# Kernel tuning notes

Measured on AMD Instinct MI355X. Metric: run time of the kernel, lower is better.

The kernel has to match this reference:

```python
import jax, jax.numpy as jnp
import numpy as np
from jax import lax

C = 256

def conv1x1(x, w, b):
    # x: [B,C,H,W], w: [O,C], b: [O]
    return jnp.einsum('bchw,oc->bohw', x, w) + b[None, :, None, None]

def conv3x3_s2(x, w, b):
    # x: [B,C,H,W], w: [O,C,3,3] -> stride 2, pad 1
    y = lax.conv_general_dilated(x, w, window_strides=(2, 2),
                                 padding=((1, 1), (1, 1)),
                                 dimension_numbers=('NCHW', 'OIHW', 'NCHW'))
    return y + b[None, :, None, None]

def to_qv(x):
    # [B,C,H,W] -> permute(0,2,3,1) -> view [B,H,W,1,C]
    return jnp.transpose(x, (0, 2, 3, 1))[:, :, :, None, :]

def to_k(x):
    # [B,C,H,W] -> permute(0,2,3,1) -> view [B,H,W,C,1]
    return jnp.transpose(x, (0, 2, 3, 1))[:, :, :, :, None]

def upsample2x_nearest(x):
    return jnp.repeat(jnp.repeat(x, 2, axis=2), 2, axis=3)


def setup_inputs() -> dict:
    key = jax.random.key(0)
    ks = jax.random.split(key, 20)
    x1 = jax.random.normal(ks[0], (2, C, 128, 128), dtype=jnp.float32)
    x2 = jax.random.normal(ks[1], (2, C, 64, 64), dtype=jnp.float32)
    s = 0.05
    d = {'x1': x1, 'x2': x2}
    names = ['q1', 'q2', 'ks1', 'ks2', 'kup', 'v1', 'v2']
    for i, n in enumerate(names):
        d[n + '_w'] = jax.random.normal(ks[2 + 2 * i], (C, C), dtype=jnp.float32) * s
        d[n + '_b'] = jax.random.normal(ks[3 + 2 * i], (C,), dtype=jnp.float32) * s
    d['kdown_w'] = jax.random.normal(ks[16], (C, C, 3, 3), dtype=jnp.float32) * s
    d['kdown_b'] = jax.random.normal(ks[17], (C,), dtype=jnp.float32) * s
    return d


def reference(x1, x2, q1_w, q1_b, q2_w, q2_b, ks1_w, ks1_b, ks2_w, ks2_b,
              kup_w, kup_b, v1_w, v1_b, v2_w, v2_b, kdown_w, kdown_b):
    q1 = to_qv(conv1x1(x1, q1_w, q1_b))            # [B,128,128,1,C]
    q2 = to_qv(conv1x1(x2, q2_w, q2_b))            # [B,64,64,1,C]
    k_up = to_k(upsample2x_nearest(conv1x1(x2, kup_w, kup_b)))  # [B,128,128,C,1]
    k_self_1 = to_k(conv1x1(x1, ks1_w, ks1_b))     # [B,128,128,C,1]
    k_self_2 = to_k(conv1x1(x2, ks2_w, ks2_b))     # [B,64,64,C,1]
    k_down = to_k(conv3x3_s2(x1, kdown_w, kdown_b))  # [B,64,64,C,1]
    v1 = to_qv(conv1x1(x1, v1_w, v1_b))            # [B,128,128,1,C]
    v2 = to_qv(conv1x1(x2, v2_w, v2_b))            # [B,64,64,1,C]
    return (q1, q2, k_up, k_self_1, k_self_2, k_down, v1, v2)
```

## Files before the change

### kernel.cpp

```cpp
#include <hip/hip_runtime.h>
#include <hip/hip_bf16.h>
#include <stdint.h>


typedef __attribute__((ext_vector_type(8))) __bf16 bf16x8;
typedef __attribute__((ext_vector_type(4))) float f32x4;

typedef const __attribute__((address_space(1))) uint32_t* gptr_t;
typedef __attribute__((address_space(3))) uint32_t* lptr_t;

__device__ __forceinline__ void cp16(void* lds, const void* g) {
  gptr_t gp = reinterpret_cast<gptr_t>(reinterpret_cast<uintptr_t>(g));
  lptr_t lp = reinterpret_cast<lptr_t>(
      static_cast<uint32_t>(reinterpret_cast<uintptr_t>(lds)));
  __builtin_amdgcn_global_load_lds(gp, lp, 16, 0, 0);
}

__global__ void nchw2nhwc_bf16(const float* __restrict__ src,
                               uint16_t* __restrict__ dst,
                               int H, int W, int pad) {
  __shared__ float tile[64][65];
  const int tid = threadIdx.x;
  const int tx = tid & 63;
  const int tg = tid >> 6;
  const int b = blockIdx.z / H;
  const int h = blockIdx.z - b * H;
  const int wt = blockIdx.x * 64;
  const int ct = blockIdx.y * 64;
  const float* s = src + ((long)(b * 256 + ct) * H + h) * W + wt;
  const long cstride = (long)H * W;
#pragma unroll
  for (int i = 0; i < 16; i++) {
    const int cl = tg * 16 + i;
    tile[cl][tx] = s[(long)cl * cstride + tx];
  }
  __syncthreads();
  const int Wp = W + 2 * pad;
  __hip_bfloat16* d = reinterpret_cast<__hip_bfloat16*>(dst);
  const long dbase =
      (((long)(b * (H + 2 * pad) + h + pad)) * Wp + pad + wt) * 256 + ct + tx;
#pragma unroll
  for (int j = 0; j < 16; j++) {
    const int wl = tg * 16 + j;
    d[dbase + (long)wl * 256] = __float2bfloat16(tile[tx][wl]);
  }
}

struct WArgs {
  const float* w1[7];
  const float* kdw;
};

__global__ void convert_weights(WArgs a, uint16_t* __restrict__ wb,
                                uint16_t* __restrict__ wt) {
  const int idx = blockIdx.x * 256 + threadIdx.x;
  if (idx < 7 * 65536) {
    const int which = idx >> 16;
    reinterpret_cast<__hip_bfloat16*>(wb)[idx] =
        __float2bfloat16(a.w1[which][idx & 65535]);
  }
  if (idx < 9 * 65536) {
    const int tap = idx >> 16;
    const int o = (idx >> 8) & 255;
    const int c = idx & 255;
    reinterpret_cast<__hip_bfloat16*>(wt)[idx] =
        __float2bfloat16(a.kdw[o * 2304 + c * 9 + tap]);
  }
}

struct Job {
  const uint16_t* A;
  const uint16_t* W;
  const float* bias;
  float* out;
  int mtiles;
  int mode;
};
struct JobArgs {
  Job j[8];
};

__global__ __launch_bounds__(256, 2) void fused_gemm(JobArgs args) {
  const Job jb = args.j[blockIdx.z];
  if ((int)blockIdx.x >= jb.mtiles) return;
  const int mtile = blockIdx.x;
  const int ntile = blockIdx.y;
  const int mode = jb.mode;

  __shared__ __align__(16) uint16_t lA[128 * 32];
  __shared__ __align__(16) uint16_t lB[128 * 32];

  const int tid = threadIdx.x;
  const int lane = tid & 63;
  const int wave = tid >> 6;
  const int wr = wave & 1;
  const int wc = wave >> 1;

  const int cid0 = wave * 128 + lane;
  const int cid1 = cid0 + 64;
  const int rA0 = cid0 >> 2, kc0 = cid0 & 3;
  const int rA1 = cid1 >> 2, kc1 = cid1 & 3;

  long abase0, abase1;
  {
    const int m0 = mtile * 128 + rA0;
    const int m1 = mtile * 128 + rA1;
    if (mode == 0) {
      abase0 = ((long)((m0 >> 14) * 130 + ((m0 >> 7) & 127) + 1) * 130 +
                (m0 & 127) + 1) * 256;
      abase1 = ((long)((m1 >> 14) * 130 + ((m1 >> 7) & 127) + 1) * 130 +
                (m1 & 127) + 1) * 256;
    } else if (mode == 3) {
      abase0 = ((long)((m0 >> 12) * 130 + 2 * ((m0 >> 6) & 63)) * 130 +
                2 * (m0 & 63)) * 256;
      abase1 = ((long)((m1 >> 12) * 130 + 2 * ((m1 >> 6) & 63)) * 130 +
                2 * (m1 & 63)) * 256;
    } else {
      abase0 = (long)m0 * 256;
      abase1 = (long)m1 * 256;
    }
  }
  const uint16_t* pa0 = jb.A + abase0 + kc0 * 8;
  const uint16_t* pa1 = jb.A + abase1 + kc1 * 8;
  const uint16_t* pb0 = jb.W + (long)(ntile * 128 + rA0) * 256 + kc0 * 8;
  const uint16_t* pb1 = jb.W + (long)(ntile * 128 + rA1) * 256 + kc1 * 8;

  uint16_t* dA0 = lA + wave * 1024;
  uint16_t* dA1 = dA0 + 512;
  uint16_t* dB0 = lB + wave * 1024;
  uint16_t* dB1 = dB0 + 512;

  const int q = lane >> 4;
  const int l15 = lane & 15;
  const uint16_t* ra[4];
  const uint16_t* rb[4];
#pragma unroll
  for (int i = 0; i < 4; i++) {
    ra[i] = lA + (wr * 64 + i * 16 + l15) * 32 + q * 8;
    rb[i] = lB + (wc * 64 + i * 16 + l15) * 32 + q * 8;
  }

  f32x4 acc[4][4] = {};

  auto step = [&](int ks, bool conv) {
    long aoff, woff;
    if (conv) {
      const int tap = ks >> 3;
      const int k0 = (ks & 7) * 32;
      const int kh = tap / 3;
      const int kw = tap - kh * 3;
      aoff = (long)(kh * 130 + kw) * 256 + k0;
      woff = (long)tap * 65536 + k0;
    } else {
      aoff = woff = (long)ks * 32;
    }
    __syncthreads();
    cp16(dA0, pa0 + aoff);
    cp16(dA1, pa1 + aoff);
    cp16(dB0, pb0 + woff);
    cp16(dB1, pb1 + woff);
    __syncthreads();
    bf16x8 af[4], bfr[4];
#pragma unroll
    for (int i = 0; i < 4; i++) af[i] = *(const bf16x8*)ra[i];
#pragma unroll
    for (int i = 0; i < 4; i++) bfr[i] = *(const bf16x8*)rb[i];
#pragma unroll
    for (int i = 0; i < 4; i++)
#pragma unroll
      for (int j = 0; j < 4; j++)
        acc[i][j] = __builtin_amdgcn_mfma_f32_16x16x32_bf16(af[i], bfr[j],
                                                            acc[i][j], 0, 0, 0);
  };

  if (mode == 3) {
    for (int ks = 0; ks < 72; ks++) step(ks, true);
  } else {
#pragma unroll
    for (int ks = 0; ks < 8; ks++) step(ks, false);
  }

  const int nbase = ntile * 128 + wc * 64 + l15;
  const int mbase = mtile * 128 + wr * 64 + q * 4;
#pragma unroll
  for (int j = 0; j < 4; j++) {
    const int n = nbase + j * 16;
    const float bv = jb.bias[n];
#pragma unroll
    for (int i = 0; i < 4; i++) {
      const int m0 = mbase + i * 16;
      const f32x4 v = acc[i][j];
      if (mode == 2) {
#pragma unroll
        for (int r = 0; r < 4; r++) {
          const int m = m0 + r;
          const int b = m >> 12;
          const int h2 = (m >> 6) & 63;
          const int w2 = m & 63;
          const float val = v[r] + bv;
          float* o = jb.out + ((long)(b * 128 + 2 * h2) * 128 + 2 * w2) * 256 + n;
          o[0] = val;
          o[256] = val;
          o[32768] = val;
          o[32768 + 256] = val;
        }
      } else {
#pragma unroll
        for (int r = 0; r < 4; r++) {
          jb.out[(long)(m0 + r) * 256 + n] = v[r] + bv;
        }
      }
    }
  }
}

extern "C" void kernel_launch(void* const* d_in, const int* in_sizes, int n_in,
                              void* d_out, int out_size, void* d_ws,
                              size_t ws_size, hipStream_t stream) {
  (void)in_sizes; (void)n_in; (void)out_size; (void)ws_size;
  const float* x1 = (const float*)d_in[0];
  const float* x2 = (const float*)d_in[1];
  float* out = (float*)d_out;

  uint16_t* x1p = (uint16_t*)d_ws;
  uint16_t* x2b = x1p + 8652800;
  uint16_t* wb = x2b + 2097152;
  uint16_t* wt = wb + 7 * 65536;

  hipMemsetAsync(x1p, 0, 8652800 * sizeof(uint16_t), stream);
  nchw2nhwc_bf16<<<dim3(2, 4, 256), 256, 0, stream>>>(x1, x1p, 128, 128, 1);
  nchw2nhwc_bf16<<<dim3(1, 4, 128), 256, 0, stream>>>(x2, x2b, 64, 64, 0);

  WArgs wa;
  wa.w1[0] = (const float*)d_in[2];
  wa.w1[1] = (const float*)d_in[4];
  wa.w1[2] = (const float*)d_in[6];
  wa.w1[3] = (const float*)d_in[8];
  wa.w1[4] = (const float*)d_in[10];
  wa.w1[5] = (const float*)d_in[12];
  wa.w1[6] = (const float*)d_in[14];
  wa.kdw = (const float*)d_in[16];
  convert_weights<<<2304, 256, 0, stream>>>(wa, wb, wt);

  JobArgs ja;
  ja.j[0] = {x1p, wt,             (const float*)d_in[17], out + 29360128L, 64, 3};
  ja.j[1] = {x1p, wb + 0 * 65536, (const float*)d_in[3],  out + 0L,        256, 0};
  ja.j[2] = {x1p, wb + 2 * 65536, (const float*)d_in[7],  out + 18874368L, 256, 0};
  ja.j[3] = {x1p, wb + 5 * 65536, (const float*)d_in[13], out + 31457280L, 256, 0};
  ja.j[4] = {x2b, wb + 4 * 65536, (const float*)d_in[11], out + 10485760L, 64, 2};
  ja.j[5] = {x2b, wb + 1 * 65536, (const float*)d_in[5],  out + 8388608L,  64, 1};
  ja.j[6] = {x2b, wb + 3 * 65536, (const float*)d_in[9],  out + 27262976L, 64, 1};
  ja.j[7] = {x2b, wb + 6 * 65536, (const float*)d_in[15], out + 39845888L, 64, 1};
  fused_gemm<<<dim3(256, 2, 8), 256, 0, stream>>>(ja);
}
```

Measured before the change: 297.3 us.

## Restructure GEMM to full-N tiles with fragment-packed weights and split-K conv

The GEMM kernel now computes a full 256-wide N tile per block, staging the whole 128x256 A tile in LDS once per tap. It reads B straight from global memory in a weight layout pre-packed into MFMA fragment order, which drops the per-32-K double barrier loop. The 3x3 stride-2 conv is split across three jobs of three taps each that atomically accumulate into an output zeroed beforehand, evening out the per-block work. The transpose and weight-conversion kernels are also vectorised with float4 loads and 16-byte stores. The cost is twice the accumulator registers and 64KB of LDS, which may lower occupancy, plus fp32 atomics on the conv output.

```diff
diff --git a/kernel.cpp b/kernel.cpp
--- a/kernel.cpp
+++ b/kernel.cpp
@@ -5,6 +5,7 @@
 
 typedef __attribute__((ext_vector_type(8))) __bf16 bf16x8;
 typedef __attribute__((ext_vector_type(4))) float f32x4;
+typedef __attribute__((ext_vector_type(8))) unsigned short u16x8;
 
 typedef const __attribute__((address_space(1))) uint32_t* gptr_t;
 typedef __attribute__((address_space(3))) uint32_t* lptr_t;
@@ -16,33 +17,43 @@
   __builtin_amdgcn_global_load_lds(gp, lp, 16, 0, 0);
 }
 
-__global__ void nchw2nhwc_bf16(const float* __restrict__ src,
-                               uint16_t* __restrict__ dst,
-                               int H, int W, int pad) {
+__global__ void nchw2nhwc_v2(const float* __restrict__ src,
+                             uint16_t* __restrict__ dst,
+                             int H, int W, int pad) {
   __shared__ float tile[64][65];
   const int tid = threadIdx.x;
-  const int tx = tid & 63;
-  const int tg = tid >> 6;
   const int b = blockIdx.z / H;
   const int h = blockIdx.z - b * H;
   const int wt = blockIdx.x * 64;
   const int ct = blockIdx.y * 64;
+  const long cs = (long)H * W;
   const float* s = src + ((long)(b * 256 + ct) * H + h) * W + wt;
-  const long cstride = (long)H * W;
-#pragma unroll
-  for (int i = 0; i < 16; i++) {
-    const int cl = tg * 16 + i;
-    tile[cl][tx] = s[(long)cl * cstride + tx];
+  const int rw = tid >> 4;
+  const int rf = tid & 15;
+#pragma unroll
+  for (int p = 0; p < 4; p++) {
+    const int cl = p * 16 + rw;
+    const float4 v = *(const float4*)(s + (long)cl * cs + rf * 4);
+    tile[cl][rf * 4 + 0] = v.x;
+    tile[cl][rf * 4 + 1] = v.y;
+    tile[cl][rf * 4 + 2] = v.z;
+    tile[cl][rf * 4 + 3] = v.w;
   }
   __syncthreads();
+  const int wl0 = tid >> 3;
+  const int cg = tid & 7;
   const int Wp = W + 2 * pad;
-  __hip_bfloat16* d = reinterpret_cast<__hip_bfloat16*>(dst);
-  const long dbase =
-      (((long)(b * (H + 2 * pad) + h + pad)) * Wp + pad + wt) * 256 + ct + tx;
-#pragma unroll
-  for (int j = 0; j < 16; j++) {
-    const int wl = tg * 16 + j;
-    d[dbase + (long)wl * 256] = __float2bfloat16(tile[tx][wl]);
+  const long rowb = ((long)(b * (H + 2 * pad) + h + pad)) * Wp + pad + wt;
+#pragma unroll
+  for (int p = 0; p < 2; p++) {
+    const int wl = p * 32 + wl0;
+    u16x8 u;
+#pragma unroll
+    for (int k = 0; k < 8; k++) {
+      __hip_bfloat16 hb = __float2bfloat16(tile[cg * 8 + k][wl]);
+      u[k] = *reinterpret_cast<uint16_t*>(&hb);
+    }
+    *(u16x8*)(dst + (rowb + wl) * 256 + ct + cg * 8) = u;
   }
 }
 
@@ -51,164 +62,172 @@
   const float* kdw;
 };
 
-__global__ void convert_weights(WArgs a, uint16_t* __restrict__ wb,
-                                uint16_t* __restrict__ wt) {
+__global__ void convert_weights_v2(WArgs a, uint16_t* __restrict__ wf) {
   const int idx = blockIdx.x * 256 + threadIdx.x;
-  if (idx < 7 * 65536) {
-    const int which = idx >> 16;
-    reinterpret_cast<__hip_bfloat16*>(wb)[idx] =
-        __float2bfloat16(a.w1[which][idx & 65535]);
-  }
-  if (idx < 9 * 65536) {
-    const int tap = idx >> 16;
-    const int o = (idx >> 8) & 255;
-    const int c = idx & 255;
-    reinterpret_cast<__hip_bfloat16*>(wt)[idx] =
-        __float2bfloat16(a.kdw[o * 2304 + c * 9 + tap]);
-  }
+  const int mat = idx >> 13;
+  const int g = idx & 8191;
+  const int jg = g >> 9;
+  const int kc = (g >> 6) & 7;
+  const int lane = g & 63;
+  const int o = jg * 16 + (lane & 15);
+  const int k0 = kc * 32 + (lane >> 4) * 8;
+  float f[8];
+  if (mat < 7) {
+    const float* w = a.w1[mat];
+    const float4 v0 = *(const float4*)(w + o * 256 + k0);
+    const float4 v1 = *(const float4*)(w + o * 256 + k0 + 4);
+    f[0] = v0.x; f[1] = v0.y; f[2] = v0.z; f[3] = v0.w;
+    f[4] = v1.x; f[5] = v1.y; f[6] = v1.z; f[7] = v1.w;
+  } else {
+    const int tap = mat - 7;
+#pragma unroll
+    for (int e = 0; e < 8; e++)
+      f[e] = a.kdw[(long)o * 2304 + (long)(k0 + e) * 9 + tap];
+  }
+  u16x8 u;
+#pragma unroll
+  for (int e = 0; e < 8; e++) {
+    __hip_bfloat16 hb = __float2bfloat16(f[e]);
+    u[e] = *reinterpret_cast<uint16_t*>(&hb);
+  }
+  *(u16x8*)(wf + (long)idx * 8) = u;
 }
 
 struct Job {
   const uint16_t* A;
-  const uint16_t* W;
+  const uint16_t* Wf;
   const float* bias;
   float* out;
   int mtiles;
   int mode;
+  int tap0;
 };
 struct JobArgs {
-  Job j[8];
+  Job j[10];
 };
 
 __global__ __launch_bounds__(256, 2) void fused_gemm(JobArgs args) {
   const Job jb = args.j[blockIdx.z];
   if ((int)blockIdx.x >= jb.mtiles) return;
   const int mtile = blockIdx.x;
-  const int ntile = blockIdx.y;
   const int mode = jb.mode;
 
-  __shared__ __align__(16) uint16_t lA[128 * 32];
-  __shared__ __align__(16) uint16_t lB[128 * 32];
+  __shared__ __align__(16) uint16_t lA[32768];
 
   const int tid = threadIdx.x;
   const int lane = tid & 63;
   const int wave = tid >> 6;
   const int wr = wave & 1;
   const int wc = wave >> 1;
-
-  const int cid0 = wave * 128 + lane;
-  const int cid1 = cid0 + 64;
-  const int rA0 = cid0 >> 2, kc0 = cid0 & 3;
-  const int rA1 = cid1 >> 2, kc1 = cid1 & 3;
-
-  long abase0, abase1;
-  {
-    const int m0 = mtile * 128 + rA0;
-    const int m1 = mtile * 128 + rA1;
-    if (mode == 0) {
-      abase0 = ((long)((m0 >> 14) * 130 + ((m0 >> 7) & 127) + 1) * 130 +
-                (m0 & 127) + 1) * 256;
-      abase1 = ((long)((m1 >> 14) * 130 + ((m1 >> 7) & 127) + 1) * 130 +
-                (m1 & 127) + 1) * 256;
-    } else if (mode == 3) {
-      abase0 = ((long)((m0 >> 12) * 130 + 2 * ((m0 >> 6) & 63)) * 130 +
-                2 * (m0 & 63)) * 256;
-      abase1 = ((long)((m1 >> 12) * 130 + 2 * ((m1 >> 6) & 63)) * 130 +
-                2 * (m1 & 63)) * 256;
-    } else {
-      abase0 = (long)m0 * 256;
-      abase1 = (long)m1 * 256;
-    }
-  }
-  const uint16_t* pa0 = jb.A + abase0 + kc0 * 8;
-  const uint16_t* pa1 = jb.A + abase1 + kc1 * 8;
-  const uint16_t* pb0 = jb.W + (long)(ntile * 128 + rA0) * 256 + kc0 * 8;
-  const uint16_t* pb1 = jb.W + (long)(ntile * 128 + rA1) * 256 + kc1 * 8;
-
-  uint16_t* dA0 = lA + wave * 1024;
-  uint16_t* dA1 = dA0 + 512;
-  uint16_t* dB0 = lB + wave * 1024;
-  uint16_t* dB1 = dB0 + 512;
-
   const int q = lane >> 4;
   const int l15 = lane & 15;
-  const uint16_t* ra[4];
-  const uint16_t* rb[4];
-#pragma unroll
-  for (int i = 0; i < 4; i++) {
-    ra[i] = lA + (wr * 64 + i * 16 + l15) * 32 + q * 8;
-    rb[i] = lB + (wc * 64 + i * 16 + l15) * 32 + q * 8;
-  }
-
-  f32x4 acc[4][4] = {};
-
-  auto step = [&](int ks, bool conv) {
-    long aoff, woff;
-    if (conv) {
-      const int tap = ks >> 3;
-      const int k0 = (ks & 7) * 32;
+
+  const uint16_t* rowA[2];
+  {
+    const int rbase = wave * 16 + (lane >> 2);
+#pragma unroll
+    for (int rh = 0; rh < 2; rh++) {
+      const int m = mtile * 128 + rh * 64 + rbase;
+      long p;
+      if (mode == 0) {
+        p = ((long)((m >> 14) * 130 + ((m >> 7) & 127) + 1)) * 130 + (m & 127) + 1;
+      } else if (mode == 3) {
+        p = ((long)((m >> 12) * 130 + 2 * ((m >> 6) & 63))) * 130 + 2 * (m & 63);
+      } else {
+        p = m;
+      }
+      rowA[rh] = jb.A + p * 256 + (lane & 3) * 8;
+    }
+  }
+
+  f32x4 acc[4][8] = {};
+  const int ntaps = (mode == 3) ? 3 : 1;
+
+  for (int t = 0; t < ntaps; t++) {
+    long aoff = 0;
+    const uint16_t* wf = jb.Wf;
+    if (mode == 3) {
+      const int tap = jb.tap0 + t;
       const int kh = tap / 3;
       const int kw = tap - kh * 3;
-      aoff = (long)(kh * 130 + kw) * 256 + k0;
-      woff = (long)tap * 65536 + k0;
-    } else {
-      aoff = woff = (long)ks * 32;
+      aoff = (long)(kh * 130 + kw) * 256;
+      wf = jb.Wf + (long)tap * 65536;
+    }
+    if (t) __syncthreads();
+#pragma unroll
+    for (int kap = 0; kap < 16; kap++) {
+      const uint16_t* src = rowA[kap & 1] + aoff + (kap >> 1) * 32;
+      cp16(lA + (kap * 256 + wave * 64) * 8, src);
     }
     __syncthreads();
-    cp16(dA0, pa0 + aoff);
-    cp16(dA1, pa1 + aoff);
-    cp16(dB0, pb0 + woff);
-    cp16(dB1, pb1 + woff);
-    __syncthreads();
-    bf16x8 af[4], bfr[4];
-#pragma unroll
-    for (int i = 0; i < 4; i++) af[i] = *(const bf16x8*)ra[i];
-#pragma unroll
-    for (int i = 0; i < 4; i++) bfr[i] = *(const bf16x8*)rb[i];
-#pragma unroll
-    for (int i = 0; i < 4; i++)
-#pragma unroll
-      for (int j = 0; j < 4; j++)
-        acc[i][j] = __builtin_amdgcn_mfma_f32_16x16x32_bf16(af[i], bfr[j],
-                                                            acc[i][j], 0, 0, 0);
-  };
-
+
+#pragma unroll
+    for (int kc = 0; kc < 8; kc++) {
+      bf16x8 av[4];
+#pragma unroll
+      for (int i = 0; i < 4; i++)
+        av[i] = *(const bf16x8*)(lA + (kc * 128 + wr * 64 + i * 16 + l15) * 32 + q * 8);
+#pragma unroll
+      for (int j = 0; j < 8; j++) {
+        const bf16x8 bv =
+            *(const bf16x8*)(wf + ((long)((wc * 8 + j) * 8 + kc) * 64 + lane) * 8);
+#pragma unroll
+        for (int i = 0; i < 4; i++)
+          acc[i][j] = __builtin_amdgcn_mfma_f32_16x16x32_bf16(av[i], bv,
+                                                              acc[i][j], 0, 0, 0);
+      }
+    }
+  }
+
+  const int nb = wc * 128 + l15;
+  const int mb = mtile * 128 + wr * 64 + q * 4;
   if (mode == 3) {
-    for (int ks = 0; ks < 72; ks++) step(ks, true);
-  } else {
-#pragma unroll
-    for (int ks = 0; ks < 8; ks++) step(ks, false);
-  }
-
-  const int nbase = ntile * 128 + wc * 64 + l15;
-  const int mbase = mtile * 128 + wr * 64 + q * 4;
-#pragma unroll
-  for (int j = 0; j < 4; j++) {
-    const int n = nbase + j * 16;
-    const float bv = jb.bias[n];
-#pragma unroll
-    for (int i = 0; i < 4; i++) {
-      const int m0 = mbase + i * 16;
-      const f32x4 v = acc[i][j];
-      if (mode == 2) {
+#pragma unroll
+    for (int j = 0; j < 8; j++) {
+      const int n = nb + j * 16;
+      const float bv = jb.bias ? jb.bias[n] : 0.0f;
+#pragma unroll
+      for (int i = 0; i < 4; i++) {
+        const int m0 = mb + i * 16;
+#pragma unroll
+        for (int r = 0; r < 4; r++)
+          atomicAdd(jb.out + (long)(m0 + r) * 256 + n, acc[i][j][r] + bv);
+      }
+    }
+  } else if (mode == 2) {
+#pragma unroll
+    for (int j = 0; j < 8; j++) {
+      const int n = nb + j * 16;
+      const float bv = jb.bias[n];
+#pragma unroll
+      for (int i = 0; i < 4; i++) {
+        const int m0 = mb + i * 16;
 #pragma unroll
         for (int r = 0; r < 4; r++) {
           const int m = m0 + r;
           const int b = m >> 12;
           const int h2 = (m >> 6) & 63;
           const int w2 = m & 63;
-          const float val = v[r] + bv;
+          const float val = acc[i][j][r] + bv;
           float* o = jb.out + ((long)(b * 128 + 2 * h2) * 128 + 2 * w2) * 256 + n;
           o[0] = val;
           o[256] = val;
           o[32768] = val;
           o[32768 + 256] = val;
         }
-      } else {
-#pragma unroll
-        for (int r = 0; r < 4; r++) {
-          jb.out[(long)(m0 + r) * 256 + n] = v[r] + bv;
-        }
+      }
+    }
+  } else {
+#pragma unroll
+    for (int j = 0; j < 8; j++) {
+      const int n = nb + j * 16;
+      const float bv = jb.bias[n];
+#pragma unroll
+      for (int i = 0; i < 4; i++) {
+        const int m0 = mb + i * 16;
+#pragma unroll
+        for (int r = 0; r < 4; r++)
+          jb.out[(long)(m0 + r) * 256 + n] = acc[i][j][r] + bv;
       }
     }
   }
@@ -224,12 +243,13 @@
 
   uint16_t* x1p = (uint16_t*)d_ws;
   uint16_t* x2b = x1p + 8652800;
-  uint16_t* wb = x2b + 2097152;
-  uint16_t* wt = wb + 7 * 65536;
+  uint16_t* wf = x2b + 2097152;
 
   hipMemsetAsync(x1p, 0, 8652800 * sizeof(uint16_t), stream);
-  nchw2nhwc_bf16<<<dim3(2, 4, 256), 256, 0, stream>>>(x1, x1p, 128, 128, 1);
-  nchw2nhwc_bf16<<<dim3(1, 4, 128), 256, 0, stream>>>(x2, x2b, 64, 64, 0);
+  hipMemsetAsync(out + 29360128L, 0, 2097152 * sizeof(float), stream);
+
+  nchw2nhwc_v2<<<dim3(2, 4, 256), 256, 0, stream>>>(x1, x1p, 128, 128, 1);
+  nchw2nhwc_v2<<<dim3(1, 4, 128), 256, 0, stream>>>(x2, x2b, 64, 64, 0);
 
   WArgs wa;
   wa.w1[0] = (const float*)d_in[2];
@@ -240,16 +260,19 @@
   wa.w1[5] = (const float*)d_in[12];
   wa.w1[6] = (const float*)d_in[14];
   wa.kdw = (const float*)d_in[16];
-  convert_weights<<<2304, 256, 0, stream>>>(wa, wb, wt);
-
+  convert_weights_v2<<<512, 256, 0, stream>>>(wa, wf);
+
+  const uint16_t* wfk = wf + 7 * 65536;
   JobArgs ja;
-  ja.j[0] = {x1p, wt,             (const float*)d_in[17], out + 29360128L, 64, 3};
-  ja.j[1] = {x1p, wb + 0 * 65536, (const float*)d_in[3],  out + 0L,        256, 0};
-  ja.j[2] = {x1p, wb + 2 * 65536, (const float*)d_in[7],  out + 18874368L, 256, 0};
-  ja.j[3] = {x1p, wb + 5 * 65536, (const float*)d_in[13], out + 31457280L, 256, 0};
-  ja.j[4] = {x2b, wb + 4 * 65536, (const float*)d_in[11], out + 10485760L, 64, 2};
-  ja.j[5] = {x2b, wb + 1 * 65536, (const float*)d_in[5],  out + 8388608L,  64, 1};
-  ja.j[6] = {x2b, wb + 3 * 65536, (const float*)d_in[9],  out + 27262976L, 64, 1};
-  ja.j[7] = {x2b, wb + 6 * 65536, (const float*)d_in[15], out + 39845888L, 64, 1};
-  fused_gemm<<<dim3(256, 2, 8), 256, 0, stream>>>(ja);
-}
+  ja.j[0] = {x1p, wfk, (const float*)d_in[17], out + 29360128L, 64, 3, 0};
+  ja.j[1] = {x1p, wfk, nullptr,                out + 29360128L, 64, 3, 3};
+  ja.j[2] = {x1p, wfk, nullptr,                out + 29360128L, 64, 3, 6};
+  ja.j[3] = {x1p, wf + 0 * 65536, (const float*)d_in[3],  out + 0L,        256, 0, 0};
+  ja.j[4] = {x1p, wf + 2 * 65536, (const float*)d_in[7],  out + 18874368L, 256, 0, 0};
+  ja.j[5] = {x1p, wf + 5 * 65536, (const float*)d_in[13], out + 31457280L, 256, 0, 0};
+  ja.j[6] = {x2b, wf + 4 * 65536, (const float*)d_in[11], out + 10485760L, 64, 2, 0};
+  ja.j[7] = {x2b, wf + 1 * 65536, (const float*)d_in[5],  out + 8388608L,  64, 1, 0};
+  ja.j[8] = {x2b, wf + 3 * 65536, (const float*)d_in[9],  out + 27262976L, 64, 1, 0};
+  ja.j[9] = {x2b, wf + 6 * 65536, (const float*)d_in[15], out + 39845888L, 64, 1, 0};
+  fused_gemm<<<dim3(256, 1, 10), 256, 0, stream>>>(ja);
+}
```

Measured after the change: 299.1 us. No clear change (+0.6%).
